# Kernel tuning notes

Hardware: AMD Instinct MI355X
Metric: run time of the kernel (lower is better)

The kernel has to match this reference:

```python
import jax, jax.numpy as jnp
from jax import lax
import numpy as np

C = 768      # embed_dim
H = 8        # num_heads
SR = 2       # sr_ratio
EPS = 1e-5


def setup_inputs() -> dict:
    key = jax.random.key(0)
    ks = jax.random.split(key, 8)
    B, n = 1, 24
    N = n ** 3  # 13824
    s = 0.02
    x = jax.random.normal(ks[0], (B, N, C), jnp.float32)
    wq = jax.random.normal(ks[1], (C, C), jnp.float32) * s          # query (no bias)
    wkv = jax.random.normal(ks[2], (C, 2 * C), jnp.float32) * s     # key_value (no bias)
    sr_w = jax.random.normal(ks[3], (C, C, SR, SR, SR), jnp.float32) * s  # Conv3d OIDHW
    sr_b = jax.random.normal(ks[4], (C,), jnp.float32) * s
    ln_g = jnp.ones((C,), jnp.float32)
    ln_b = jnp.zeros((C,), jnp.float32)
    proj_w = jax.random.normal(ks[5], (C, C), jnp.float32) * s
    proj_b = jax.random.normal(ks[6], (C,), jnp.float32) * s
    return {"x": x, "wq": wq, "wkv": wkv, "sr_w": sr_w, "sr_b": sr_b,
            "ln_g": ln_g, "ln_b": ln_b, "proj_w": proj_w, "proj_b": proj_b}


def reference(x, wq, wkv, sr_w, sr_b, ln_g, ln_b, proj_w, proj_b):
    B, N, Cdim = x.shape
    d = Cdim // H
    n = round(N ** (1.0 / 3.0))
    # q: [B,H,N,d]
    q = (x @ wq).reshape(B, N, H, d).transpose(0, 2, 1, 3)
    # spatial reduction: conv3d with kernel=stride=SR
    x_ = x.transpose(0, 2, 1).reshape(B, Cdim, n, n, n)
    x_ = lax.conv_general_dilated(x_, sr_w, (SR, SR, SR), 'VALID',
                                  dimension_numbers=('NCDHW', 'OIDHW', 'NCDHW'))
    x_ = x_ + sr_b[None, :, None, None, None]
    x_ = x_.reshape(B, Cdim, -1).transpose(0, 2, 1)  # [B, N', C]
    mu = x_.mean(-1, keepdims=True)
    var = x_.var(-1, keepdims=True)
    x_ = (x_ - mu) / jnp.sqrt(var + EPS) * ln_g + ln_b
    # kv: [2,B,H,N',d]
    kv = (x_ @ wkv).reshape(B, -1, 2, H, d).transpose(2, 0, 3, 1, 4)
    k, v = kv[0], kv[1]
    # NOTE: original scales by sqrt(num_heads), not sqrt(head_dim) -- kept faithfully.
    scores = jnp.einsum('bhqd,bhkd->bhqk', q, k) / jnp.sqrt(jnp.float32(H))
    probs = jax.nn.softmax(scores, axis=-1)
    out = jnp.einsum('bhqk,bhkd->bhqd', probs, v)
    out = out.transpose(0, 2, 1, 3).reshape(B, N, Cdim)
    return out @ proj_w + proj_b
```

## Files before the change

### kernel.cpp

```cpp
#include <hip/hip_runtime.h>
#include <hip/hip_bf16.h>

typedef __hip_bfloat16 bf16;
typedef unsigned short u16;

#define CD 768
#define HH 8
#define HD 96
#define NT 13824
#define NR 1728
#define KCONV 6144
#define NRCD 1327104L

typedef __attribute__((ext_vector_type(8))) __bf16 bf16x8;
typedef __attribute__((ext_vector_type(8))) unsigned short us8;
typedef __attribute__((ext_vector_type(4))) unsigned short us4;
typedef __attribute__((ext_vector_type(4))) float floatx4;

#define OFF_XB   0L
#define OFF_Q    21233664L
#define OFF_XR   42467328L
#define OFF_XLN  47775744L
#define OFF_WQT  50429952L
#define OFF_WKVT 51609600L
#define OFF_PRJT 53968896L
#define OFF_SRWR 55148544L
#define OFF_PRB  64587264L

__device__ __forceinline__ float b2f(bf16 v) { return __bfloat162float(v); }
__device__ __forceinline__ floatx4 mfma16(bf16x8 a, bf16x8 b, floatx4 c) {
    return __builtin_amdgcn_mfma_f32_16x16x32_bf16(a, b, c, 0, 0, 0);
}
__device__ __forceinline__ u16 f2bf_bits(float x) {
    return __builtin_bit_cast(u16, __float2bfloat16(x));
}
__device__ __forceinline__ float ldin(const void* p, long i, int bf) {
    return bf ? b2f(((const bf16*)p)[i]) : ((const float*)p)[i];
}
__device__ __forceinline__ int probe_bf(const void* lng) {
    return ((const u16*)lng)[0] == 0x3F80;
}

#define GLOAD16(gp, lp) __builtin_amdgcn_global_load_lds( \
    (const __attribute__((address_space(1))) unsigned int*)(gp), \
    (__attribute__((address_space(3))) unsigned int*)(lp), 16, 0, 0)

__global__ __launch_bounds__(256) void cvt_kernel(
    const void* __restrict__ src, bf16* __restrict__ dst, long nchunk,
    const void* __restrict__ lng)
{
    const int bf = probe_bf(lng);
    long c = (long)blockIdx.x * 256 + threadIdx.x;
    if (c >= nchunk) return;
    if (bf) {
        ((us8*)dst)[c] = ((const us8*)src)[c];
    } else {
        const float* s = (const float*)src + c * 8;
        us8 o;
#pragma unroll
        for (int j = 0; j < 8; ++j) o[j] = f2bf_bits(s[j]);
        ((us8*)dst)[c] = o;
    }
}

__device__ __forceinline__ void do_trans(
    const void* __restrict__ src, bf16* __restrict__ dst, int R, int Cc,
    int bf, int bx32, int by32, int tx, int ty, float (*tile)[33])
{
    const int bx = bx32 * 32, by = by32 * 32;
#pragma unroll
    for (int rr = 0; rr < 4; ++rr)
        tile[ty + rr * 8][tx] = ldin(src, (long)(by + ty + rr * 8) * Cc + bx + tx, bf);
    __syncthreads();
#pragma unroll
    for (int rr = 0; rr < 4; ++rr)
        dst[(long)(bx + ty + rr * 8) * R + by + tx] =
            __float2bfloat16(tile[tx][ty + rr * 8]);
}

__global__ __launch_bounds__(256) void prep_kernel(
    const void* __restrict__ wq, const void* __restrict__ wkv,
    const void* __restrict__ proj_w, const void* __restrict__ sr_w,
    const void* __restrict__ proj_b, const void* __restrict__ lng,
    bf16* __restrict__ wqT, bf16* __restrict__ wkvT, bf16* __restrict__ prjT,
    bf16* __restrict__ srwR, bf16* __restrict__ prbB)
{
    __shared__ float tile[32][33];
    const int bf = probe_bf(lng);
    const int tx = threadIdx.x & 31, ty = threadIdx.x >> 5;
    const int id = blockIdx.x;
    if (id < 576) {
        do_trans(wq, wqT, CD, CD, bf, id % 24, id / 24, tx, ty, tile);
    } else if (id < 1728) {
        int j = id - 576;
        do_trans(wkv, wkvT, CD, 1536, bf, j % 48, j / 48, tx, ty, tile);
    } else if (id < 2304) {
        int j = id - 1728;
        do_trans(proj_w, prjT, CD, CD, bf, j % 24, j / 24, tx, ty, tile);
    } else if (id < 3456) {
        int j = id - 2304;
        const long total = 768L * 6144;
        for (long e = (long)j * 256 + threadIdx.x; e < total; e += 1152L * 256) {
            long o = e / 6144;
            int rem = (int)(e - o * 6144);
            int tap = rem / 768, i = rem - tap * 768;
            srwR[e] = __float2bfloat16(ldin(sr_w, o * 6144 + i * 8 + tap, bf));
        }
    } else {
        if (threadIdx.x < 96) {
            long c = threadIdx.x;
            if (bf) {
                ((us8*)prbB)[c] = ((const us8*)proj_b)[c];
            } else {
                const float* s = (const float*)proj_b + c * 8;
                us8 o;
#pragma unroll
                for (int jj = 0; jj < 8; ++jj) o[jj] = f2bf_bits(s[jj]);
                ((us8*)prbB)[c] = o;
            }
        }
    }
}

template <bool GATHER, bool BIAS, int DST, int SPLITK, bool PRESCALE>
__global__ __launch_bounds__(256) void gemm_mfma(
    const bf16* __restrict__ A, const bf16* __restrict__ Bt,
    const bf16* __restrict__ bias, void* __restrict__ C, bf16* __restrict__ C2,
    int M, int N, int K, const void* __restrict__ lng)
{
    const int bf = (DST == 0) ? probe_bf(lng) : 0;
    __shared__ alignas(16) u16 Al[2][128][32];
    __shared__ alignas(16) u16 Bl[2][128][32];
    const int tid  = threadIdx.x;
    const int wave = tid >> 6, lane = tid & 63;
    const int l15  = lane & 15, quad = lane >> 4;
    const int m0 = blockIdx.y * 128, n0 = blockIdx.x * 128;
    const int mw = (wave & 1) * 64, nw = (wave >> 1) * 64;

    const int row0 = wave * 16 + (lane >> 2);
    const int row1 = row0 + 64;
    const int cb8  = (((lane & 3) ^ ((lane >> 3) & 3)) << 3);

    int tokbase0 = 0, tokbase1 = 0;
    long arow0 = 0, arow1 = 0;
    {
        int mc0 = min(m0 + row0, M - 1);
        int mc1 = min(m0 + row1, M - 1);
        if (GATHER) {
            int zo0 = mc0 / 144, yo0 = (mc0 / 12) % 12, xo0 = mc0 % 12;
            tokbase0 = zo0 * 1152 + yo0 * 48 + xo0 * 2;
            int zo1 = mc1 / 144, yo1 = (mc1 / 12) % 12, xo1 = mc1 % 12;
            tokbase1 = zo1 * 1152 + yo1 * 48 + xo1 * 2;
        } else {
            arow0 = (long)mc0 * K;
            arow1 = (long)mc1 * K;
        }
    }
    const long brow0 = (long)(n0 + row0) * K;
    const long brow1 = (long)(n0 + row1) * K;

    floatx4 acc[4][4];
#pragma unroll
    for (int mi = 0; mi < 4; ++mi)
#pragma unroll
        for (int ni = 0; ni < 4; ++ni) acc[mi][ni] = (floatx4){0.f, 0.f, 0.f, 0.f};

    const int ksteps = K >> 5;
    const int kchunk = ksteps / SPLITK;
    const int kb0 = (SPLITK > 1) ? blockIdx.z * kchunk : 0;
    const int kbend = kb0 + kchunk;

    auto stage = [&](int kb, int c) {
        const long ko = (long)kb << 5;
        const bf16 *ga0, *ga1;
        if (GATHER) {
            int kk0 = kb << 5;
            int tap = kk0 / 768;
            int i0  = kk0 - tap * 768 + cb8;
            int toff = (tap >> 2) * 576 + ((tap >> 1) & 1) * 24 + (tap & 1);
            ga0 = A + (long)(tokbase0 + toff) * 768 + i0;
            ga1 = A + (long)(tokbase1 + toff) * 768 + i0;
        } else {
            ga0 = A + arow0 + ko + cb8;
            ga1 = A + arow1 + ko + cb8;
        }
        GLOAD16(ga0, &Al[c][wave * 16][0]);
        GLOAD16(ga1, &Al[c][64 + wave * 16][0]);
        GLOAD16(Bt + brow0 + ko + cb8, &Bl[c][wave * 16][0]);
        GLOAD16(Bt + brow1 + ko + cb8, &Bl[c][64 + wave * 16][0]);
    };

    int cur = 0;
    stage(kb0, 0);
    asm volatile("s_waitcnt vmcnt(0)" ::: "memory");
    __syncthreads();

    const int sl = ((quad ^ ((l15 >> 1) & 3)) << 3);

    for (int kb = kb0; kb < kbend; ++kb) {
        if (kb + 1 < kbend) stage(kb + 1, cur ^ 1);

        bf16x8 af[4], bfr[4];
#pragma unroll
        for (int mi = 0; mi < 4; ++mi)
            af[mi] = *(const bf16x8*)&Al[cur][mw + mi * 16 + l15][sl];
#pragma unroll
        for (int ni = 0; ni < 4; ++ni)
            bfr[ni] = *(const bf16x8*)&Bl[cur][nw + ni * 16 + l15][sl];
#pragma unroll
        for (int mi = 0; mi < 4; ++mi)
#pragma unroll
            for (int ni = 0; ni < 4; ++ni)
                acc[mi][ni] = mfma16(af[mi], bfr[ni], acc[mi][ni]);

        asm volatile("s_waitcnt vmcnt(0)" ::: "memory");
        __syncthreads();
        cur ^= 1;
    }

#pragma unroll
    for (int mi = 0; mi < 4; ++mi) {
        int rowb = m0 + mw + mi * 16 + quad * 4;
#pragma unroll
        for (int ni = 0; ni < 4; ++ni) {
            int col = n0 + nw + ni * 16 + l15;
            float bv = BIAS ? b2f(bias[col]) : 0.f;
#pragma unroll
            for (int r = 0; r < 4; ++r) {
                int row = rowb + r;
                if (row < M) {
                    float v = acc[mi][ni][r] + bv;
                    if (PRESCALE) v *= 0.35355339059327373f;
                    long idx = (long)row * N + col;
                    if (DST == 2)      ((float*)C)[idx] = v;
                    else if (DST == 1) ((bf16*)C)[idx] = __float2bfloat16(v);
                    else if (DST == 3) {
                        if (col < 768) ((bf16*)C)[(long)row * 768 + col] = __float2bfloat16(v);
                        else           C2[(long)(col - 768) * NR + row] = __float2bfloat16(v);
                    } else if (DST == 5) {
                        ((float*)C)[(long)blockIdx.z * NRCD + idx] = v;
                    } else {
                        if (bf) ((bf16*)C)[idx] = __float2bfloat16(v);
                        else    ((float*)C)[idx] = v;
                    }
                }
            }
        }
    }
}

__global__ __launch_bounds__(256) void ln_kernel(
    const float* __restrict__ Xr, const void* __restrict__ srb,
    const void* __restrict__ g, const void* __restrict__ b,
    bf16* __restrict__ Xln)
{
    const int bf = probe_bf(g);
    __shared__ float red[256];
    __shared__ float mu_s, rs_s;
    const int t = blockIdx.x, tid = threadIdx.x;
    const float* row = Xr + (long)t * CD;
    float v0 = (row[tid]              + row[NRCD + tid])
             + (row[2 * NRCD + tid]   + row[3 * NRCD + tid])       + ldin(srb, tid, bf);
    float v1 = (row[tid + 256]        + row[NRCD + tid + 256])
             + (row[2 * NRCD + tid + 256] + row[3 * NRCD + tid + 256]) + ldin(srb, tid + 256, bf);
    float v2 = (row[tid + 512]        + row[NRCD + tid + 512])
             + (row[2 * NRCD + tid + 512] + row[3 * NRCD + tid + 512]) + ldin(srb, tid + 512, bf);
    red[tid] = v0 + v1 + v2;
    __syncthreads();
    for (int off = 128; off; off >>= 1) {
        if (tid < off) red[tid] += red[tid + off];
        __syncthreads();
    }
    if (tid == 0) mu_s = red[0] * (1.0f / CD);
    __syncthreads();
    float mu = mu_s;
    float d0 = v0 - mu, d1 = v1 - mu, d2 = v2 - mu;
    red[tid] = d0 * d0 + d1 * d1 + d2 * d2;
    __syncthreads();
    for (int off = 128; off; off >>= 1) {
        if (tid < off) red[tid] += red[tid + off];
        __syncthreads();
    }
    if (tid == 0) rs_s = rsqrtf(red[0] * (1.0f / CD) + 1e-5f);
    __syncthreads();
    float rs = rs_s;
    bf16* orow = Xln + (long)t * CD;
    orow[tid]       = __float2bfloat16(d0 * rs * ldin(g, tid, bf)       + ldin(b, tid, bf));
    orow[tid + 256] = __float2bfloat16(d1 * rs * ldin(g, tid + 256, bf) + ldin(b, tid + 256, bf));
    orow[tid + 512] = __float2bfloat16(d2 * rs * ldin(g, tid + 512, bf) + ldin(b, tid + 512, bf));
}

__global__ __launch_bounds__(256, 2) void attn_mfma_kernel(
    const bf16* __restrict__ Qg, const bf16* __restrict__ Kg,
    const bf16* __restrict__ VTg, bf16* __restrict__ Og)
{
    __shared__ u16 Ks[64][104];
    __shared__ u16 Vt[96][72];
    __shared__ u16 PT[4][64][64];

    const int tid  = threadIdx.x;
    const int wave = tid >> 6;
    const int lane = tid & 63;
    const int l15  = lane & 15;
    const int quad = lane >> 4;

    const int lin  = blockIdx.y * 54 + blockIdx.x;
    const int nid  = (lin & 7) * 54 + (lin >> 3);
    const int h    = nid / 54;
    const int qblk = nid - h * 54;
    const int q0   = qblk * 256 + wave * 64;

    bf16x8 bq[4][3];
#pragma unroll
    for (int qc = 0; qc < 4; ++qc)
#pragma unroll
        for (int kc = 0; kc < 3; ++kc)
            bq[qc][kc] = *(const bf16x8*)(Qg + (long)(q0 + qc * 16 + l15) * CD
                                          + h * HD + kc * 32 + quad * 8);

    floatx4 o[4][6];
    float lp[4] = {0.f, 0.f, 0.f, 0.f};
#pragma unroll
    for (int qc = 0; qc < 4; ++qc)
#pragma unroll
        for (int dc = 0; dc < 6; ++dc) o[qc][dc] = (floatx4){0.f, 0.f, 0.f, 0.f};

    const int stok = tid >> 2;
    const int dseg = (tid & 3) * 24;
    const int vdim = tid >> 3;
    const int vt8  = (tid & 7) << 3;
    const u16* kbase = (const u16*)Kg + (long)stok * 768 + h * HD + dseg;
    const u16* vbase = (const u16*)VTg + (long)(h * HD + vdim) * NR + vt8;

    us8 kreg[3], vreg[3];
#pragma unroll
    for (int s = 0; s < 3; ++s) kreg[s] = *(const us8*)(kbase + s * 8);
#pragma unroll
    for (int i = 0; i < 3; ++i) vreg[i] = *(const us8*)(vbase + (long)i * 32 * NR);

    for (int kt = 0; kt < NR; kt += 64) {
        __syncthreads();
#pragma unroll
        for (int s = 0; s < 3; ++s) *(us8*)&Ks[stok][dseg + s * 8] = kreg[s];
#pragma unroll
        for (int i = 0; i < 3; ++i) *(us8*)&Vt[vdim + i * 32][vt8] = vreg[i];
        __syncthreads();

        if (kt + 64 < NR) {
            const u16* k2 = kbase + (long)(kt + 64) * 768;
            const u16* v2 = vbase + (kt + 64);
#pragma unroll
            for (int s = 0; s < 3; ++s) kreg[s] = *(const us8*)(k2 + s * 8);
#pragma unroll
            for (int i = 0; i < 3; ++i) vreg[i] = *(const us8*)(v2 + (long)i * 32 * NR);
        }

#pragma unroll
        for (int tc = 0; tc < 4; ++tc) {
            bf16x8 ak[3];
#pragma unroll
            for (int kc = 0; kc < 3; ++kc)
                ak[kc] = *(const bf16x8*)&Ks[tc * 16 + l15][kc * 32 + quad * 8];
#pragma unroll
            for (int qc = 0; qc < 4; ++qc) {
                floatx4 acc = {0.f, 0.f, 0.f, 0.f};
                __builtin_amdgcn_s_setprio(1);
#pragma unroll
                for (int kc = 0; kc < 3; ++kc) acc = mfma16(ak[kc], bq[qc][kc], acc);
                __builtin_amdgcn_s_setprio(0);
                float e0 = __expf(acc[0]), e1 = __expf(acc[1]);
                float e2 = __expf(acc[2]), e3 = __expf(acc[3]);
                lp[qc] += (e0 + e1) + (e2 + e3);
                us4 p4;
                p4[0] = f2bf_bits(e0); p4[1] = f2bf_bits(e1);
                p4[2] = f2bf_bits(e2); p4[3] = f2bf_bits(e3);
                const int pb = (tc * 2 + (quad >> 1)) ^ (l15 & 7);
                *(us4*)&PT[wave][qc * 16 + l15][pb * 8 + (quad & 1) * 4] = p4;
            }
        }

#pragma unroll
        for (int ks = 0; ks < 2; ++ks) {
            bf16x8 ap[4];
#pragma unroll
            for (int qc = 0; qc < 4; ++qc) {
                const int rb = (ks * 4 + quad) ^ (l15 & 7);
                ap[qc] = *(const bf16x8*)&PT[wave][qc * 16 + l15][rb * 8];
            }
            __builtin_amdgcn_s_setprio(1);
#pragma unroll
            for (int dc = 0; dc < 6; ++dc) {
                bf16x8 bv = *(const bf16x8*)&Vt[dc * 16 + l15][ks * 32 + quad * 8];
#pragma unroll
                for (int qc = 0; qc < 4; ++qc)
                    o[qc][dc] = mfma16(ap[qc], bv, o[qc][dc]);
            }
            __builtin_amdgcn_s_setprio(0);
        }
    }

#pragma unroll
    for (int qc = 0; qc < 4; ++qc) {
        float ls = lp[qc];
        ls += __shfl_xor(ls, 16);
        ls += __shfl_xor(ls, 32);
        float inv = 1.0f / ls;
#pragma unroll
        for (int r = 0; r < 4; ++r) {
            float invr = __shfl(inv, quad * 4 + r, 16);
            int row = q0 + qc * 16 + quad * 4 + r;
#pragma unroll
            for (int dc = 0; dc < 6; ++dc)
                Og[(long)row * CD + h * HD + dc * 16 + l15] =
                    __float2bfloat16(o[qc][dc][r] * invr);
        }
    }
}

extern "C" void kernel_launch(void* const* d_in, const int* in_sizes, int n_in,
                              void* d_out, int out_size, void* d_ws, size_t ws_size,
                              hipStream_t stream) {
    const void* x      = d_in[0];
    const void* wq     = d_in[1];
    const void* wkv    = d_in[2];
    const void* sr_w   = d_in[3];
    const void* sr_b   = d_in[4];
    const void* ln_g   = d_in[5];
    const void* ln_b   = d_in[6];
    const void* proj_w = d_in[7];
    const void* proj_b = d_in[8];

    char* ws = (char*)d_ws;
    bf16*  xb    = (bf16*)(ws + OFF_XB);
    bf16*  O     = (bf16*)(ws + OFF_XB);
    float* Xr4   = (float*)(ws + OFF_Q);
    bf16*  Q     = (bf16*)(ws + OFF_Q);
    bf16*  Kg    = (bf16*)(ws + OFF_XR);
    bf16*  VTg   = (bf16*)(ws + OFF_XR + 2654208);
    bf16*  Xln   = (bf16*)(ws + OFF_XLN);
    bf16*  wqT   = (bf16*)(ws + OFF_WQT);
    bf16*  wkvT  = (bf16*)(ws + OFF_WKVT);
    bf16*  prjT  = (bf16*)(ws + OFF_PRJT);
    bf16*  srwR  = (bf16*)(ws + OFF_SRWR);
    bf16*  prbB  = (bf16*)(ws + OFF_PRB);

    prep_kernel<<<3457, 256, 0, stream>>>(wq, wkv, proj_w, sr_w, proj_b, ln_g,
                                          wqT, wkvT, prjT, srwR, prbB);
    cvt_kernel<<<5184, 256, 0, stream>>>(x, xb, (long)NT * CD / 8, ln_g);

    gemm_mfma<true, false, 5, 4, false><<<dim3(6, 14, 4), 256, 0, stream>>>(
        xb, srwR, nullptr, Xr4, nullptr, NR, CD, KCONV, ln_g);
    ln_kernel<<<NR, 256, 0, stream>>>(Xr4, sr_b, ln_g, ln_b, Xln);
    gemm_mfma<false, false, 3, 1, false><<<dim3(12, 14), 256, 0, stream>>>(
        Xln, wkvT, nullptr, Kg, VTg, NR, 1536, CD, ln_g);
    gemm_mfma<false, false, 1, 1, true><<<dim3(6, 108), 256, 0, stream>>>(
        xb, wqT, nullptr, Q, nullptr, NT, CD, CD, ln_g);
    attn_mfma_kernel<<<dim3(NT / 256, HH), 256, 0, stream>>>(Q, Kg, VTg, O);
    gemm_mfma<false, true, 0, 1, false><<<dim3(6, 108), 256, 0, stream>>>(
        O, prjT, prbB, d_out, nullptr, NT, CD, CD, ln_g);
}
```

Before: 371.7 us.

## Triple-buffer GEMM LDS pipeline and fold input conversion into prep kernel

The MFMA GEMM moves from double to triple buffering in LDS. Tiles are prefetched two k-steps ahead, and each iteration waits with a partial vmcnt and a single barrier instead of a full drain plus syncthreads. This is meant to hide global-load latency better, at the cost of 50% more shared memory per block, which may lower occupancy. Separately, the x fp32-to-bf16 conversion is merged into the prep kernel as extra blocks, removing one kernel launch and letting it overlap with weight preparation.

```diff
diff --git a/kernel.cpp b/kernel.cpp
--- a/kernel.cpp
+++ b/kernel.cpp
@@ -45,24 +45,6 @@
     (const __attribute__((address_space(1))) unsigned int*)(gp), \
     (__attribute__((address_space(3))) unsigned int*)(lp), 16, 0, 0)
 
-__global__ __launch_bounds__(256) void cvt_kernel(
-    const void* __restrict__ src, bf16* __restrict__ dst, long nchunk,
-    const void* __restrict__ lng)
-{
-    const int bf = probe_bf(lng);
-    long c = (long)blockIdx.x * 256 + threadIdx.x;
-    if (c >= nchunk) return;
-    if (bf) {
-        ((us8*)dst)[c] = ((const us8*)src)[c];
-    } else {
-        const float* s = (const float*)src + c * 8;
-        us8 o;
-#pragma unroll
-        for (int j = 0; j < 8; ++j) o[j] = f2bf_bits(s[j]);
-        ((us8*)dst)[c] = o;
-    }
-}
-
 __device__ __forceinline__ void do_trans(
     const void* __restrict__ src, bf16* __restrict__ dst, int R, int Cc,
     int bf, int bx32, int by32, int tx, int ty, float (*tile)[33])
@@ -81,9 +63,10 @@
 __global__ __launch_bounds__(256) void prep_kernel(
     const void* __restrict__ wq, const void* __restrict__ wkv,
     const void* __restrict__ proj_w, const void* __restrict__ sr_w,
-    const void* __restrict__ proj_b, const void* __restrict__ lng,
+    const void* __restrict__ proj_b, const void* __restrict__ x,
+    const void* __restrict__ lng,
     bf16* __restrict__ wqT, bf16* __restrict__ wkvT, bf16* __restrict__ prjT,
-    bf16* __restrict__ srwR, bf16* __restrict__ prbB)
+    bf16* __restrict__ srwR, bf16* __restrict__ prbB, bf16* __restrict__ xb)
 {
     __shared__ float tile[32][33];
     const int bf = probe_bf(lng);
@@ -106,7 +89,7 @@
             int tap = rem / 768, i = rem - tap * 768;
             srwR[e] = __float2bfloat16(ldin(sr_w, o * 6144 + i * 8 + tap, bf));
         }
-    } else {
+    } else if (id == 3456) {
         if (threadIdx.x < 96) {
             long c = threadIdx.x;
             if (bf) {
@@ -119,6 +102,19 @@
                 ((us8*)prbB)[c] = o;
             }
         }
+    } else {
+        long c = (long)(id - 3457) * 256 + threadIdx.x;
+        if (c < (long)NT * CD / 8) {
+            if (bf) {
+                ((us8*)xb)[c] = ((const us8*)x)[c];
+            } else {
+                const float* s = (const float*)x + c * 8;
+                us8 o;
+#pragma unroll
+                for (int jj = 0; jj < 8; ++jj) o[jj] = f2bf_bits(s[jj]);
+                ((us8*)xb)[c] = o;
+            }
+        }
     }
 }
 
@@ -128,9 +124,8 @@
     const bf16* __restrict__ bias, void* __restrict__ C, bf16* __restrict__ C2,
     int M, int N, int K, const void* __restrict__ lng)
 {
-    const int bf = (DST == 0) ? probe_bf(lng) : 0;
-    __shared__ alignas(16) u16 Al[2][128][32];
-    __shared__ alignas(16) u16 Bl[2][128][32];
+    __shared__ alignas(16) u16 Al[3][128][32];
+    __shared__ alignas(16) u16 Bl[3][128][32];
     const int tid  = threadIdx.x;
     const int wave = tid >> 6, lane = tid & 63;
     const int l15  = lane & 15, quad = lane >> 4;
@@ -190,15 +185,18 @@
         GLOAD16(Bt + brow1 + ko + cb8, &Bl[c][64 + wave * 16][0]);
     };
 
-    int cur = 0;
     stage(kb0, 0);
-    asm volatile("s_waitcnt vmcnt(0)" ::: "memory");
-    __syncthreads();
+    stage(kb0 + 1, 1);
 
     const int sl = ((quad ^ ((l15 >> 1) & 3)) << 3);
 
     for (int kb = kb0; kb < kbend; ++kb) {
-        if (kb + 1 < kbend) stage(kb + 1, cur ^ 1);
+        const int cur = (kb - kb0) % 3;
+        if (kb + 1 < kbend) asm volatile("s_waitcnt vmcnt(4)" ::: "memory");
+        else                asm volatile("s_waitcnt vmcnt(0)" ::: "memory");
+        __builtin_amdgcn_s_barrier();
+        __builtin_amdgcn_sched_barrier(0);
+        if (kb + 2 < kbend) stage(kb + 2, (cur + 2) % 3);
 
         bf16x8 af[4], bfr[4];
 #pragma unroll
@@ -212,11 +210,9 @@
 #pragma unroll
             for (int ni = 0; ni < 4; ++ni)
                 acc[mi][ni] = mfma16(af[mi], bfr[ni], acc[mi][ni]);
-
-        asm volatile("s_waitcnt vmcnt(0)" ::: "memory");
-        __syncthreads();
-        cur ^= 1;
-    }
+    }
+
+    const int bf = (DST == 0) ? probe_bf(lng) : 0;
 
 #pragma unroll
     for (int mi = 0; mi < 4; ++mi) {
@@ -444,9 +440,8 @@
     bf16*  srwR  = (bf16*)(ws + OFF_SRWR);
     bf16*  prbB  = (bf16*)(ws + OFF_PRB);
 
-    prep_kernel<<<3457, 256, 0, stream>>>(wq, wkv, proj_w, sr_w, proj_b, ln_g,
-                                          wqT, wkvT, prjT, srwR, prbB);
-    cvt_kernel<<<5184, 256, 0, stream>>>(x, xb, (long)NT * CD / 8, ln_g);
+    prep_kernel<<<8641, 256, 0, stream>>>(wq, wkv, proj_w, sr_w, proj_b, x,
+                                          ln_g, wqT, wkvT, prjT, srwR, prbB, xb);
 
     gemm_mfma<true, false, 5, 4, false><<<dim3(6, 14, 4), 256, 0, stream>>>(
         xb, srwR, nullptr, Xr4, nullptr, NR, CD, KCONV, ln_g);
```

Result: no change. 371.1 us (-0.2%).
